# Kernel tuning notes

Measured on AMD Instinct MI355X. Metric: run time of the kernel, lower is better.

Reference implementation:

```python
import jax, jax.numpy as jnp
import numpy as np

DIM = 512
HEADS = 8
DIM_HEAD = 64
LANDMARKS = 256
PINV_ITERS = 6
RES_K = 33


def layernorm(x, g, b, eps=1e-5):
    mu = jnp.mean(x, -1, keepdims=True)
    var = jnp.mean((x - mu) ** 2, -1, keepdims=True)
    return (x - mu) / jnp.sqrt(var + eps) * g + b


def moore_penrose_pinv(x, iters=PINV_ITERS):
    abs_x = jnp.abs(x)
    col = abs_x.sum(-1)
    row = abs_x.sum(-2)
    z = jnp.swapaxes(x, -1, -2) / (jnp.max(col) * jnp.max(row))
    I = jnp.eye(x.shape[-1], dtype=x.dtype)
    for _ in range(iters):
        xz = x @ z
        z = 0.25 * z @ (13.0 * I - xz @ (15.0 * I - xz @ (7.0 * I - xz)))
    return z


def nystrom_attention(x, Wqkv, Wout, bout, res_w):
    b, n, _ = x.shape
    m = LANDMARKS
    pad = (m - n % m) % m
    if pad:
        x = jnp.pad(x, ((0, 0), (pad, 0), (0, 0)))  # front pad, as in lucidrains impl
    qkv = x @ Wqkv  # (b, np, 3*inner)
    q, k, v = jnp.split(qkv, 3, axis=-1)
    to_heads = lambda t: t.reshape(b, -1, HEADS, DIM_HEAD).transpose(0, 2, 1, 3)
    q, k, v = to_heads(q), to_heads(k), to_heads(v)  # (b,h,np,d)
    q = q * (DIM_HEAD ** -0.5)
    l = -(-n // m)  # ceil(n/m), tokens per landmark
    ql = q.reshape(b, HEADS, m, l, DIM_HEAD).sum(3) / l  # (b,h,m,d)
    kl = k.reshape(b, HEADS, m, l, DIM_HEAD).sum(3) / l
    sim1 = jnp.einsum('bhid,bhjd->bhij', q, kl)   # (b,h,np,m)
    sim2 = jnp.einsum('bhid,bhjd->bhij', ql, kl)  # (b,h,m,m)
    sim3 = jnp.einsum('bhid,bhjd->bhij', ql, k)   # (b,h,m,np)
    a1 = jax.nn.softmax(sim1, -1)
    a2 = jax.nn.softmax(sim2, -1)
    a3 = jax.nn.softmax(sim3, -1)
    a2_inv = moore_penrose_pinv(a2)
    out = (a1 @ a2_inv) @ (a3 @ v)  # (b,h,np,d)
    # depthwise residual conv along sequence (kernel 33x1, groups=heads, no bias)
    res = jax.lax.conv_general_dilated(
        v, res_w, (1, 1), [(RES_K // 2, RES_K // 2), (0, 0)],
        dimension_numbers=('NCHW', 'OIHW', 'NCHW'), feature_group_count=HEADS)
    out = out + res
    out = out.transpose(0, 2, 1, 3).reshape(b, -1, HEADS * DIM_HEAD)
    out = out @ Wout + bout
    return out[:, -n:]


def depthwise2d(x, w, b, pad):
    y = jax.lax.conv_general_dilated(
        x, w, (1, 1), [(pad, pad), (pad, pad)],
        dimension_numbers=('NCHW', 'OIHW', 'NCHW'), feature_group_count=DIM)
    return y + b[None, :, None, None]


def ppeg(x, H, W, w7, b7, w5, b5, w3, b3):
    B, _, C = x.shape
    cls_tok, feat = x[:, :1], x[:, 1:]
    cnn = feat.transpose(0, 2, 1).reshape(B, C, H, W)
    y = depthwise2d(cnn, w7, b7, 3) + cnn + depthwise2d(cnn, w5, b5, 2) + depthwise2d(cnn, w3, b3, 1)
    y = y.reshape(B, C, H * W).transpose(0, 2, 1)
    return jnp.concatenate([cls_tok, y], axis=1)


def setup_inputs() -> dict:
    key = jax.random.key(0)
    ks = jax.random.split(key, 20)
    s = 0.02
    n_classes = 5
    inp = {
        'data': jax.random.normal(ks[0], (1, 15000, 1024), jnp.float32),
        'W_fc1': jax.random.normal(ks[1], (1024, DIM), jnp.float32) * s,
        'b_fc1': jnp.zeros((DIM,), jnp.float32),
        'cls_token': jax.random.normal(ks[2], (1, 1, DIM), jnp.float32),
        'ln1_g': jnp.ones((DIM,), jnp.float32), 'ln1_b': jnp.zeros((DIM,), jnp.float32),
        'qkv1': jax.random.normal(ks[3], (DIM, 3 * HEADS * DIM_HEAD), jnp.float32) * s,
        'out1_w': jax.random.normal(ks[4], (HEADS * DIM_HEAD, DIM), jnp.float32) * s,
        'out1_b': jnp.zeros((DIM,), jnp.float32),
        'res1': jax.random.normal(ks[5], (HEADS, 1, RES_K, 1), jnp.float32) * s,
        'w7': jax.random.normal(ks[6], (DIM, 1, 7, 7), jnp.float32) * s,
        'b7': jnp.zeros((DIM,), jnp.float32),
        'w5': jax.random.normal(ks[7], (DIM, 1, 5, 5), jnp.float32) * s,
        'b5': jnp.zeros((DIM,), jnp.float32),
        'w3': jax.random.normal(ks[8], (DIM, 1, 3, 3), jnp.float32) * s,
        'b3': jnp.zeros((DIM,), jnp.float32),
        'ln2_g': jnp.ones((DIM,), jnp.float32), 'ln2_b': jnp.zeros((DIM,), jnp.float32),
        'qkv2': jax.random.normal(ks[9], (DIM, 3 * HEADS * DIM_HEAD), jnp.float32) * s,
        'out2_w': jax.random.normal(ks[10], (HEADS * DIM_HEAD, DIM), jnp.float32) * s,
        'out2_b': jnp.zeros((DIM,), jnp.float32),
        'res2': jax.random.normal(ks[11], (HEADS, 1, RES_K, 1), jnp.float32) * s,
        'norm_g': jnp.ones((DIM,), jnp.float32), 'norm_b': jnp.zeros((DIM,), jnp.float32),
        'W_fc2': jax.random.normal(ks[12], (DIM, n_classes), jnp.float32) * s,
        'b_fc2': jnp.zeros((n_classes,), jnp.float32),
    }
    return inp


def reference(data, W_fc1, b_fc1, cls_token, ln1_g, ln1_b, qkv1, out1_w, out1_b, res1,
              w7, b7, w5, b5, w3, b3, ln2_g, ln2_b, qkv2, out2_w, out2_b, res2,
              norm_g, norm_b, W_fc2, b_fc2):
    h = jax.nn.relu(data @ W_fc1 + b_fc1)  # (B, N, 512)
    N = h.shape[1]
    _H = int(np.ceil(np.sqrt(N)))
    _W = _H
    add = _H * _W - N
    h = jnp.concatenate([h, h[:, :add]], axis=1)  # pad to square grid
    B = h.shape[0]
    h = jnp.concatenate([jnp.broadcast_to(cls_token, (B, 1, DIM)), h], axis=1)
    h = h + nystrom_attention(layernorm(h, ln1_g, ln1_b), qkv1, out1_w, out1_b, res1)
    h = ppeg(h, _H, _W, w7, b7, w5, b5, w3, b3)
    h = h + nystrom_attention(layernorm(h, ln2_g, ln2_b), qkv2, out2_w, out2_b, res2)
    h = layernorm(h, norm_g, norm_b)[:, 0]
    logits = h @ W_fc2 + b_fc2
    Y_prob = jax.nn.softmax(logits, -1)
    Y_hat = jnp.argmax(logits, -1)
    return logits, Y_prob, Y_hat
```

## Files before the change

### kernel.cpp

```cpp
#include <hip/hip_runtime.h>
#include <math.h>

#define NP 15360
#define NPQ 15488
#define NTOK 15130
#define HG 123

typedef __attribute__((ext_vector_type(8))) short s8b;
typedef __attribute__((ext_vector_type(4))) float f4;

__device__ inline float bf2f(ushort u) { return __uint_as_float(((unsigned)u) << 16); }
__device__ inline ushort f2bf(float f) {
    unsigned u = __float_as_uint(f);
    unsigned r = (u + 0x7fffu + ((u >> 16) & 1u)) >> 16;
    return (ushort)r;
}

__global__ __launch_bounds__(256)
void gemm_f32(const float* __restrict__ A, int lda, long sA,
              const float* __restrict__ B, int ldb, long sB,
              float* __restrict__ C, int ldc, long sC,
              int M, int N, int K,
              const float* __restrict__ bias,
              const float* __restrict__ E, int ldE, long sE, float eS,
              float cS, int relu, int accum)
{
    A += (long)blockIdx.z * sA;
    B += (long)blockIdx.z * sB;
    C += (long)blockIdx.z * sC;
    if (E) E += (long)blockIdx.z * sE;
    const int m0 = blockIdx.y * 64, n0 = blockIdx.x * 64;
    const int t = threadIdx.x;
    const int tx = t & 15, ty = t >> 4;
    __shared__ float As[16][64];
    __shared__ float Bs[16][64];
    float acc[4][4] = {};
    const int arow = t >> 2, akc = (t & 3) * 4;
    const int brow = t >> 4, bnc = (t & 15) * 4;
    for (int k0 = 0; k0 < K; k0 += 16) {
        float4 av = make_float4(0.f, 0.f, 0.f, 0.f);
        if (m0 + arow < M) av = *(const float4*)(A + (long)(m0 + arow) * lda + k0 + akc);
        As[akc + 0][arow] = av.x; As[akc + 1][arow] = av.y;
        As[akc + 2][arow] = av.z; As[akc + 3][arow] = av.w;
        float4 bv = *(const float4*)(B + (long)(k0 + brow) * ldb + n0 + bnc);
        *(float4*)&Bs[brow][bnc] = bv;
        __syncthreads();
#pragma unroll
        for (int kk = 0; kk < 16; ++kk) {
            float4 a4 = *(const float4*)&As[kk][ty * 4];
            float4 b4 = *(const float4*)&Bs[kk][tx * 4];
            float a[4] = {a4.x, a4.y, a4.z, a4.w};
            float b[4] = {b4.x, b4.y, b4.z, b4.w};
#pragma unroll
            for (int i = 0; i < 4; i++)
#pragma unroll
                for (int j = 0; j < 4; j++) acc[i][j] = fmaf(a[i], b[j], acc[i][j]);
        }
        __syncthreads();
    }
#pragma unroll
    for (int i = 0; i < 4; i++) {
        int m = m0 + ty * 4 + i;
        if (m < M) {
#pragma unroll
            for (int j = 0; j < 4; j++) {
                int n = n0 + tx * 4 + j;
                float v = cS * acc[i][j];
                if (E) v = fmaf(eS, E[(long)m * ldE + n], v);
                if (bias) v += bias[n];
                if (relu) v = fmaxf(v, 0.f);
                if (accum) C[(long)m * ldc + n] += v;
                else C[(long)m * ldc + n] = v;
            }
        }
    }
}

template<int MT, int NT, int WROWS, int WCOLS>
__global__ __launch_bounds__(256)
void gemm_mfma(const ushort* __restrict__ A, int lda, long sA,
               const ushort* __restrict__ Bt, int ldb, long sB,
               float* __restrict__ C, int ldc, long sC,
               int M, int K,
               const float* __restrict__ bias, int relu, int accum)
{
    constexpr int TM = MT * 16 * WROWS;
    constexpr int TN = NT * 16 * WCOLS;
    constexpr int BKP = 40;
    constexpr int AIT = TM / 64;
    constexpr int BIT = TN / 64;
    __shared__ ushort As[TM * BKP];
    __shared__ ushort Bs[TN * BKP];
    A  += (long)blockIdx.z * sA;
    Bt += (long)blockIdx.z * sB;
    C  += (long)blockIdx.z * sC;
    const int t = threadIdx.x;
    const int nwg = gridDim.x * gridDim.y;
    const int flat = blockIdx.y * gridDim.x + blockIdx.x;
    const int q8 = nwg >> 3, r8 = nwg & 7;
    const int xcd = flat & 7, idx = flat >> 3;
    const int swz = (xcd < r8) ? (xcd * (q8 + 1) + idx)
                               : (r8 * (q8 + 1) + (xcd - r8) * q8 + idx);
    const int m0 = (swz / gridDim.x) * TM;
    const int n0 = (swz % gridDim.x) * TN;
    const int w = t >> 6, l = t & 63;
    const int wm = (w / WCOLS) * (MT * 16), wn = (w % WCOLS) * (NT * 16);
    const int lr = l & 15;
    const int lk = (l >> 4) * 8;
    const int srow = t >> 2, skc = (t & 3) * 8;
    f4 acc[MT][NT] = {};
    s8b pa[AIT], pb[BIT];
#pragma unroll
    for (int i = 0; i < AIT; i++)
        pa[i] = *(const s8b*)(A + (long)(m0 + srow + i * 64) * lda + skc);
#pragma unroll
    for (int i = 0; i < BIT; i++)
        pb[i] = *(const s8b*)(Bt + (long)(n0 + srow + i * 64) * ldb + skc);
    for (int k0 = 0; k0 < K; k0 += 32) {
        __syncthreads();
#pragma unroll
        for (int i = 0; i < AIT; i++)
            *(s8b*)(&As[(srow + i * 64) * BKP + skc]) = pa[i];
#pragma unroll
        for (int i = 0; i < BIT; i++)
            *(s8b*)(&Bs[(srow + i * 64) * BKP + skc]) = pb[i];
        if (k0 + 32 < K) {
#pragma unroll
            for (int i = 0; i < AIT; i++)
                pa[i] = *(const s8b*)(A + (long)(m0 + srow + i * 64) * lda + k0 + 32 + skc);
#pragma unroll
            for (int i = 0; i < BIT; i++)
                pb[i] = *(const s8b*)(Bt + (long)(n0 + srow + i * 64) * ldb + k0 + 32 + skc);
        }
        __syncthreads();
        s8b af[MT], bf[NT];
#pragma unroll
        for (int i = 0; i < MT; i++) af[i] = *(const s8b*)(&As[(wm + i * 16 + lr) * BKP + lk]);
#pragma unroll
        for (int j = 0; j < NT; j++) bf[j] = *(const s8b*)(&Bs[(wn + j * 16 + lr) * BKP + lk]);
#pragma unroll
        for (int i = 0; i < MT; i++)
#pragma unroll
            for (int j = 0; j < NT; j++)
                acc[i][j] = __builtin_amdgcn_mfma_f32_16x16x32_bf16(af[i], bf[j], acc[i][j], 0, 0, 0);
    }
    const int orow = (l >> 4) * 4;
#pragma unroll
    for (int i = 0; i < MT; i++) {
#pragma unroll
        for (int r = 0; r < 4; r++) {
            int m = m0 + wm + i * 16 + orow + r;
            if (m < M) {
#pragma unroll
                for (int j = 0; j < NT; j++) {
                    int n = n0 + wn + j * 16 + lr;
                    float vv = acc[i][j][r];
                    if (bias) vv += bias[n];
                    if (relu) vv = fmaxf(vv, 0.f);
                    if (accum) C[(long)m * ldc + n] += vv;
                    else C[(long)m * ldc + n] = vv;
                }
            }
        }
    }
}

__global__ __launch_bounds__(256)
void gemm_nn16(const ushort* __restrict__ A, const ushort* __restrict__ B,
               const ushort* __restrict__ E, ushort* __restrict__ C,
               int N, int K, float cS, float eS, long sAB)
{
    __shared__ ushort As[64 * 40];
    __shared__ ushort Bs[64 * 40];
    A += (long)blockIdx.z * sAB;
    B += (long)blockIdx.z * sAB;
    if (E) E += (long)blockIdx.z * sAB;
    C += (long)blockIdx.z * sAB;
    const int t = threadIdx.x;
    const int m0 = blockIdx.y * 64, n0 = blockIdx.x * 64;
    const int w = t >> 6, l = t & 63;
    const int wm = (w >> 1) * 32, wn = (w & 1) * 32;
    const int lr = l & 15, lk = (l >> 4) * 8;
    f4 acc[2][2] = {};
    for (int k0 = 0; k0 < K; k0 += 32) {
        {
            int row = t >> 2, kc = (t & 3) * 8;
            s8b v = *(const s8b*)(A + (long)(m0 + row) * K + k0 + kc);
            *(s8b*)(&As[row * 40 + kc]) = v;
            int kk = t >> 3, nc = (t & 7) * 8;
            s8b vb = *(const s8b*)(B + (long)(k0 + kk) * N + n0 + nc);
#pragma unroll
            for (int j = 0; j < 8; j++) Bs[(nc + j) * 40 + kk] = ((ushort*)&vb)[j];
        }
        __syncthreads();
        s8b af[2], bf[2];
#pragma unroll
        for (int i = 0; i < 2; i++) af[i] = *(const s8b*)(&As[(wm + i * 16 + lr) * 40 + lk]);
#pragma unroll
        for (int j = 0; j < 2; j++) bf[j] = *(const s8b*)(&Bs[(wn + j * 16 + lr) * 40 + lk]);
#pragma unroll
        for (int i = 0; i < 2; i++)
#pragma unroll
            for (int j = 0; j < 2; j++)
                acc[i][j] = __builtin_amdgcn_mfma_f32_16x16x32_bf16(af[i], bf[j], acc[i][j], 0, 0, 0);
        __syncthreads();
    }
    const int orow = (l >> 4) * 4;
#pragma unroll
    for (int i = 0; i < 2; i++)
#pragma unroll
        for (int r = 0; r < 4; r++) {
            int m = m0 + wm + i * 16 + orow + r;
#pragma unroll
            for (int j = 0; j < 2; j++) {
                int n = n0 + wn + j * 16 + lr;
                float vv = cS * acc[i][j][r];
                if (E) vv = fmaf(eS, bf2f(E[(long)m * N + n]), vv);
                C[(long)m * N + n] = f2bf(vv);
            }
        }
}

__global__ __launch_bounds__(256)
void gemm_qkv_mfma(const ushort* __restrict__ A, const ushort* __restrict__ Bt,
                   ushort* __restrict__ qo, ushort* __restrict__ ko, ushort* __restrict__ vo)
{
    constexpr int BKP = 40;
    __shared__ ushort As[128 * BKP];
    __shared__ ushort Bs[128 * BKP];
    const int t = threadIdx.x;
    const int nwg = gridDim.x * gridDim.y;
    const int flat = blockIdx.y * gridDim.x + blockIdx.x;
    const int q8 = nwg >> 3, r8 = nwg & 7;
    const int xcd = flat & 7, idx = flat >> 3;
    const int swz = (xcd < r8) ? (xcd * (q8 + 1) + idx)
                               : (r8 * (q8 + 1) + (xcd - r8) * q8 + idx);
    const int m0 = (swz / gridDim.x) * 128;
    const int n0 = (swz % gridDim.x) * 128;
    const int w = t >> 6, l = t & 63;
    const int wm = (w >> 1) * 64, wn = (w & 1) * 64;
    const int lr = l & 15;
    const int lk = (l >> 4) * 8;
    const int srow = t >> 2, skc = (t & 3) * 8;
    f4 acc[4][4] = {};
    s8b pa[2], pb[2];
#pragma unroll
    for (int i = 0; i < 2; i++) {
        pa[i] = *(const s8b*)(A + (long)(m0 + srow + i * 64) * 512 + skc);
        pb[i] = *(const s8b*)(Bt + (long)(n0 + srow + i * 64) * 512 + skc);
    }
    for (int k0 = 0; k0 < 512; k0 += 32) {
        __syncthreads();
#pragma unroll
        for (int i = 0; i < 2; i++) {
            *(s8b*)(&As[(srow + i * 64) * BKP + skc]) = pa[i];
            *(s8b*)(&Bs[(srow + i * 64) * BKP + skc]) = pb[i];
        }
        if (k0 + 32 < 512) {
#pragma unroll
            for (int i = 0; i < 2; i++) {
                pa[i] = *(const s8b*)(A + (long)(m0 + srow + i * 64) * 512 + k0 + 32 + skc);
                pb[i] = *(const s8b*)(Bt + (long)(n0 + srow + i * 64) * 512 + k0 + 32 + skc);
            }
        }
        __syncthreads();
        s8b af[4], bf[4];
#pragma unroll
        for (int i = 0; i < 4; i++) af[i] = *(const s8b*)(&As[(wm + i * 16 + lr) * BKP + lk]);
#pragma unroll
        for (int j = 0; j < 4; j++) bf[j] = *(const s8b*)(&Bs[(wn + j * 16 + lr) * BKP + lk]);
#pragma unroll
        for (int i = 0; i < 4; i++)
#pragma unroll
            for (int j = 0; j < 4; j++)
                acc[i][j] = __builtin_amdgcn_mfma_f32_16x16x32_bf16(af[i], bf[j], acc[i][j], 0, 0, 0);
    }
    const int orow = (l >> 4) * 4;
#pragma unroll
    for (int i = 0; i < 4; i++) {
#pragma unroll
        for (int r = 0; r < 4; r++) {
            int m = m0 + wm + i * 16 + orow + r;
#pragma unroll
            for (int j = 0; j < 4; j++) {
                int col = n0 + wn + j * 16 + lr;
                int which = col >> 9, h = (col >> 6) & 7, d = col & 63;
                float vv = acc[i][j][r];
                if (which == 0) vv *= 0.125f;
                ushort* dst = which == 0 ? qo : (which == 1 ? ko : vo);
                dst[((long)h * NPQ + m) * 64 + d] = f2bf(vv);
            }
        }
    }
}

__global__ __launch_bounds__(256, 3)
void k_flash_a3v(const ushort* __restrict__ qlb, const ushort* __restrict__ kg,
                 const ushort* __restrict__ vg,
                 float* __restrict__ pacc, float* __restrict__ pml)
{
    const int c = blockIdx.x;
    const int qt = blockIdx.y;
    const int h = blockIdx.z;
    const int t = threadIdx.x;
    const int w = t >> 6, lane = t & 63;
    const int quad = lane >> 4, l16 = lane & 15;
    const s8b vones = {0x3F80, 0x3F80, 0x3F80, 0x3F80, 0x3F80, 0x3F80, 0x3F80, 0x3F80};

    __shared__ union {
        struct { ushort Vt[64][40]; ushort Ps[128][40]; } s;
        float Os[128][68];
    } L;

    s8b aq[2][2];
    const ushort* qbase = qlb + ((long)h * 256 + qt * 128 + w * 32) * 64;
#pragma unroll
    for (int mi = 0; mi < 2; mi++)
#pragma unroll
        for (int kf = 0; kf < 2; kf++)
            aq[mi][kf] = *(const s8b*)(qbase + (mi * 16 + l16) * 64 + kf * 32 + quad * 8);

    f4 oacc[2][4] = {};
    f4 lacc[2] = {};

    const ushort* kh = kg + (long)h * NPQ * 64;
    const ushort* vh = vg + (long)h * NPQ * 64;
    const int key0c = c * 256;

    const int vkk = (t >> 3) & 31;
    const int vdc = (t & 7) * 8;
    const int vcolp = (vkk + ((vdc >> 3) & 3) * 8) & 31;

    s8b vvN = *(const s8b*)(vh + (long)(key0c + vkk) * 64 + vdc);
    s8b bqN[2][2];
#pragma unroll
    for (int nj = 0; nj < 2; nj++)
#pragma unroll
        for (int kf = 0; kf < 2; kf++)
            bqN[nj][kf] = *(const s8b*)(kh + (long)(key0c + nj * 16 + l16) * 64 + kf * 32 + quad * 8);

#pragma unroll
    for (int sub = 0; sub < 8; sub++) {
        int key0 = key0c + sub * 32;
        s8b vvC = vvN;
        s8b bq[2][2];
#pragma unroll
        for (int nj = 0; nj < 2; nj++)
#pragma unroll
            for (int kf = 0; kf < 2; kf++) bq[nj][kf] = bqN[nj][kf];
        if (sub < 7) {
            vvN = *(const s8b*)(vh + (long)(key0 + 32 + vkk) * 64 + vdc);
#pragma unroll
            for (int nj = 0; nj < 2; nj++)
#pragma unroll
                for (int kf = 0; kf < 2; kf++)
                    bqN[nj][kf] = *(const s8b*)(kh + (long)(key0 + 32 + nj * 16 + l16) * 64 + kf * 32 + quad * 8);
        }
        __syncthreads();
        {
#pragma unroll
            for (int j = 0; j < 8; j++) L.s.Vt[vdc + j][vcolp] = ((ushort*)&vvC)[j];
        }
        f4 sacc[2][2] = {};
#pragma unroll
        for (int mi = 0; mi < 2; mi++)
#pragma unroll
            for (int nj = 0; nj < 2; nj++) {
                sacc[mi][nj] = __builtin_amdgcn_mfma_f32_16x16x32_bf16(aq[mi][0], bq[nj][0], sacc[mi][nj], 0, 0, 0);
                sacc[mi][nj] = __builtin_amdgcn_mfma_f32_16x16x32_bf16(aq[mi][1], bq[nj][1], sacc[mi][nj], 0, 0, 0);
            }
#pragma unroll
        for (int mi = 0; mi < 2; mi++)
#pragma unroll
            for (int r = 0; r < 4; r++) {
                int row = w * 32 + mi * 16 + quad * 4 + r;
                L.s.Ps[row][l16]      = f2bf(__expf(sacc[mi][0][r]));
                L.s.Ps[row][16 + l16] = f2bf(__expf(sacc[mi][1][r]));
            }
        __syncthreads();
        s8b ap[2], bv[4];
#pragma unroll
        for (int mi = 0; mi < 2; mi++)
            ap[mi] = *(const s8b*)(&L.s.Ps[w * 32 + mi * 16 + l16][quad * 8]);
#pragma unroll
        for (int dj = 0; dj < 4; dj++) {
            int d = dj * 16 + l16;
            int rot = (d >> 3) & 3;
            int cb = ((quad + rot) & 3) * 8;
            bv[dj] = *(const s8b*)(&L.s.Vt[d][cb]);
        }
#pragma unroll
        for (int mi = 0; mi < 2; mi++) {
#pragma unroll
            for (int dj = 0; dj < 4; dj++)
                oacc[mi][dj] = __builtin_amdgcn_mfma_f32_16x16x32_bf16(ap[mi], bv[dj], oacc[mi][dj], 0, 0, 0);
            lacc[mi] = __builtin_amdgcn_mfma_f32_16x16x32_bf16(ap[mi], vones, lacc[mi], 0, 0, 0);
        }
    }
    __syncthreads();
#pragma unroll
    for (int mi = 0; mi < 2; mi++)
#pragma unroll
        for (int dj = 0; dj < 4; dj++)
#pragma unroll
            for (int r = 0; r < 4; r++)
                L.Os[w * 32 + mi * 16 + quad * 4 + r][dj * 16 + l16] = oacc[mi][dj][r];
    long pbase = (long)(h * 60 + c);
    if (l16 == 0) {
#pragma unroll
        for (int mi = 0; mi < 2; mi++)
#pragma unroll
            for (int r = 0; r < 4; r++) {
                int i = qt * 128 + w * 32 + mi * 16 + quad * 4 + r;
                pml[pbase * 512 + i] = 0.f;
                pml[pbase * 512 + 256 + i] = lacc[mi][r];
            }
    }
    __syncthreads();
    float* pc = pacc + pbase * 16384 + qt * 128;
    int d = t >> 2, ig = t & 3;
#pragma unroll
    for (int u = 0; u < 8; u++) {
        int i0 = ig * 32 + u * 4;
        float4 v4 = make_float4(L.Os[i0][d], L.Os[i0 + 1][d], L.Os[i0 + 2][d], L.Os[i0 + 3][d]);
        *(float4*)(pc + (long)d * 256 + i0) = v4;
    }
}

__global__ __launch_bounds__(256, 3)
void k_attn1(const ushort* __restrict__ qg, const ushort* __restrict__ klb,
             const ushort* __restrict__ BmT, const ushort* __restrict__ vg,
             const float* __restrict__ rw, ushort* __restrict__ ohb)
{
    const int m0 = blockIdx.x * 128;
    const int h = blockIdx.y;
    const int t = threadIdx.x;
    const int w = t >> 6, lane = t & 63;
    const int quad = lane >> 4, l16 = lane & 15;
    const s8b vones = {0x3F80, 0x3F80, 0x3F80, 0x3F80, 0x3F80, 0x3F80, 0x3F80, 0x3F80};

    __shared__ union {
        ushort Ps[2][128][40];
        ushort Os[128][68];
    } L;
    __shared__ __attribute__((aligned(16))) ushort Vs[160][64];

    const ushort* vh = vg + (long)h * NPQ * 64;
    {
        const ushort* srcw = vh + (long)(214 + m0 + w * 40) * 64 + lane * 8;
        ushort* dstw = &Vs[w * 40][0];
#pragma unroll
        for (int it = 0; it < 5; it++)
            __builtin_amdgcn_global_load_lds(
                (const __attribute__((address_space(1))) void*)(srcw + it * 512),
                (__attribute__((address_space(3))) void*)(dstw + it * 512),
                16, 0, 0);
    }

    s8b aq[2][2];
    const ushort* qbase = qg + ((long)h * NPQ + 230 + m0 + w * 32) * 64;
#pragma unroll
    for (int mi = 0; mi < 2; mi++)
#pragma unroll
        for (int kf = 0; kf < 2; kf++)
            aq[mi][kf] = *(const s8b*)(qbase + (mi * 16 + l16) * 64 + kf * 32 + quad * 8);

    const ushort* kh = klb + (long)h * 16384;
    const ushort* bmt = BmT + (long)h * 16384;

    s8b bqN[2][2];
#pragma unroll
    for (int nj = 0; nj < 2; nj++)
#pragma unroll
        for (int kf = 0; kf < 2; kf++)
            bqN[nj][kf] = *(const s8b*)(kh + (long)(nj * 16 + l16) * 64 + kf * 32 + quad * 8);

    f4 oacc[2][4] = {};
    f4 lacc[2] = {};
#pragma unroll
    for (int sub = 0; sub < 8; sub++) {
        int key0 = sub * 32;
        s8b bq[2][2];
#pragma unroll
        for (int nj = 0; nj < 2; nj++)
#pragma unroll
            for (int kf = 0; kf < 2; kf++) bq[nj][kf] = bqN[nj][kf];
        if (sub < 7) {
#pragma unroll
            for (int nj = 0; nj < 2; nj++)
#pragma unroll
                for (int kf = 0; kf < 2; kf++)
                    bqN[nj][kf] = *(const s8b*)(kh + (long)(key0 + 32 + nj * 16 + l16) * 64 + kf * 32 + quad * 8);
        }
        s8b bv[4];
#pragma unroll
        for (int dj = 0; dj < 4; dj++)
            bv[dj] = *(const s8b*)(bmt + (long)(dj * 16 + l16) * 256 + key0 + quad * 8);
        f4 sacc[2][2] = {};
#pragma unroll
        for (int mi = 0; mi < 2; mi++)
#pragma unroll
            for (int nj = 0; nj < 2; nj++) {
                sacc[mi][nj] = __builtin_amdgcn_mfma_f32_16x16x32_bf16(aq[mi][0], bq[nj][0], sacc[mi][nj], 0, 0, 0);
                sacc[mi][nj] = __builtin_amdgcn_mfma_f32_16x16x32_bf16(aq[mi][1], bq[nj][1], sacc[mi][nj], 0, 0, 0);
            }
        int par = sub & 1;
#pragma unroll
        for (int mi = 0; mi < 2; mi++)
#pragma unroll
            for (int r = 0; r < 4; r++) {
                int row = w * 32 + mi * 16 + quad * 4 + r;
                L.Ps[par][row][l16]      = f2bf(__expf(sacc[mi][0][r]));
                L.Ps[par][row][16 + l16] = f2bf(__expf(sacc[mi][1][r]));
            }
        s8b ap[2];
#pragma unroll
        for (int mi = 0; mi < 2; mi++)
            ap[mi] = *(const s8b*)(&L.Ps[par][w * 32 + mi * 16 + l16][quad * 8]);
#pragma unroll
        for (int mi = 0; mi < 2; mi++) {
#pragma unroll
            for (int dj = 0; dj < 4; dj++)
                oacc[mi][dj] = __builtin_amdgcn_mfma_f32_16x16x32_bf16(ap[mi], bv[dj], oacc[mi][dj], 0, 0, 0);
            lacc[mi] = __builtin_amdgcn_mfma_f32_16x16x32_bf16(ap[mi], vones, lacc[mi], 0, 0, 0);
        }
    }
    __syncthreads();

    if (214 + m0 + 160 > NP) {
        for (int r = w * 32; r < w * 32 + 64 && r < 160; ++r)
            if (214 + m0 + r >= NP) Vs[r][lane] = 0;
    }

#pragma unroll
    for (int mi = 0; mi < 2; mi++)
#pragma unroll
        for (int r = 0; r < 4; r++) {
            float inv = 1.f / lacc[mi][r];
            int row = w * 32 + mi * 16 + quad * 4 + r;
#pragma unroll
            for (int dj = 0; dj < 4; dj++)
                L.Os[row][dj * 16 + l16] = f2bf(oacc[mi][dj][r] * inv);
        }
    float rwf[33];
#pragma unroll
    for (int kk = 0; kk < 33; kk++) rwf[kk] = rw[h * 33 + kk];
#pragma unroll
    for (int half = 0; half < 2; half++) {
        const int rbase = w * 32 + half * 16;
        float vr[48];
#pragma unroll
        for (int s = 0; s < 48; s++) vr[s] = bf2f(Vs[rbase + s][lane]);
        float conv[16];
#pragma unroll
        for (int i = 0; i < 16; i++) conv[i] = 0.f;
#pragma unroll
        for (int kk = 0; kk < 33; kk++) {
            float wk = rwf[kk];
#pragma unroll
            for (int i = 0; i < 16; i++) conv[i] = fmaf(wk, vr[i + kk], conv[i]);
        }
        int t0 = m0 + rbase;
#pragma unroll
        for (int i = 0; i < 16; i++) {
            int tk = t0 + i;
            if (tk < NTOK) {
                float val = bf2f(L.Os[rbase + i][lane]) + conv[i];
                ohb[(long)tk * 512 + h * 64 + lane] = f2bf(val);
            }
        }
    }
}

__global__ __launch_bounds__(256)
void k_layernorm(const float* __restrict__ h, ushort* __restrict__ xln,
                 const float* __restrict__ g, const float* __restrict__ b, int pad)
{
    int row = blockIdx.x, t = threadIdx.x;
    if (row < pad) {
        xln[(long)row * 512 + t] = 0;
        xln[(long)row * 512 + t + 256] = 0;
        return;
    }
    const float* src = h + (long)(row - pad) * 512;
    float x1 = src[t], x2 = src[t + 256];
    float s = x1 + x2, q = x1 * x1 + x2 * x2;
    __shared__ float rs[4], rq[4], st[2];
    int wid = t >> 6, lane = t & 63;
#pragma unroll
    for (int o = 32; o > 0; o >>= 1) { s += __shfl_down(s, o); q += __shfl_down(q, o); }
    if (lane == 0) { rs[wid] = s; rq[wid] = q; }
    __syncthreads();
    if (t == 0) {
        float S = rs[0] + rs[1] + rs[2] + rs[3];
        float Q = rq[0] + rq[1] + rq[2] + rq[3];
        float mean = S / 512.f;
        float var = Q / 512.f - mean * mean;
        st[0] = mean; st[1] = rsqrtf(var + 1e-5f);
    }
    __syncthreads();
    float mean = st[0], rstd = st[1];
    xln[(long)row * 512 + t] = f2bf((x1 - mean) * rstd * g[t] + b[t]);
    xln[(long)row * 512 + t + 256] = f2bf((x2 - mean) * rstd * g[t + 256] + b[t + 256]);
}

__global__ __launch_bounds__(256)
void k_padcls(float* __restrict__ hbuf, const float* __restrict__ cls)
{
    int i = blockIdx.x, t = threadIdx.x;
    if (i == 0) { hbuf[t] = cls[t]; hbuf[t + 256] = cls[t + 256]; }
    else {
        hbuf[(long)(15000 + i) * 512 + t] = hbuf[(long)i * 512 + t];
        hbuf[(long)(15000 + i) * 512 + t + 256] = hbuf[(long)i * 512 + t + 256];
    }
}

__global__ __launch_bounds__(256)
void k_wT(const float* __restrict__ Wm, ushort* __restrict__ Wt, int K, int N, long sW, long sWt)
{
    Wm += (long)blockIdx.z * sW; Wt += (long)blockIdx.z * sWt;
    __shared__ float tile[32][33];
    int tx = threadIdx.x & 31, ty = threadIdx.x >> 5;
    int n0 = blockIdx.x * 32, k0 = blockIdx.y * 32;
#pragma unroll
    for (int u = 0; u < 4; u++) tile[ty + u * 8][tx] = Wm[(long)(k0 + ty + u * 8) * N + n0 + tx];
    __syncthreads();
#pragma unroll
    for (int u = 0; u < 4; u++) Wt[(long)(n0 + ty + u * 8) * K + k0 + tx] = f2bf(tile[tx][ty + u * 8]);
}

__global__ __launch_bounds__(256)
void k_cvt(const float4* __restrict__ src, ushort4* __restrict__ dst, long n4)
{
    long i = (long)blockIdx.x * 256 + threadIdx.x;
    if (i < n4) {
        float4 v = src[i];
        ushort4 o;
        o.x = f2bf(v.x); o.y = f2bf(v.y); o.z = f2bf(v.z); o.w = f2bf(v.w);
        dst[i] = o;
    }
}

__global__ __launch_bounds__(256)
void k_b2f(const ushort4* __restrict__ src, float4* __restrict__ dst, long n4)
{
    long i = (long)blockIdx.x * 256 + threadIdx.x;
    if (i < n4) {
        ushort4 v = src[i];
        dst[i] = make_float4(bf2f(v.x), bf2f(v.y), bf2f(v.z), bf2f(v.w));
    }
}

__global__ __launch_bounds__(64)
void k_landmarks(const ushort* __restrict__ q, const ushort* __restrict__ k,
                 float* __restrict__ ql, ushort* __restrict__ qlb,
                 float* __restrict__ klT, ushort* __restrict__ klb,
                 unsigned* __restrict__ scal)
{
    int i = blockIdx.x, h = blockIdx.y, d = threadIdx.x;
    if (i == 0 && h == 0 && d == 0) { scal[0] = 0u; scal[1] = 0u; }
    long base = ((long)h * NPQ + (long)i * 60) * 64 + d;
    float sq = 0.f, sk = 0.f;
    for (int j = 0; j < 60; j++) { sq += bf2f(q[base + j * 64]); sk += bf2f(k[base + j * 64]); }
    float qv = sq / 60.f, kv = sk / 60.f;
    ql[((long)h * 256 + i) * 64 + d] = qv;
    qlb[((long)h * 256 + i) * 64 + d] = f2bf(qv);
    klT[((long)h * 64 + d) * 256 + i] = kv;
    klb[((long)h * 256 + i) * 64 + d] = f2bf(kv);
}

__global__ __launch_bounds__(256)
void k_softmax256(float* __restrict__ X, ushort* __restrict__ X16, long headStride)
{
    float* row = X + (long)blockIdx.y * headStride + (long)blockIdx.x * 256;
    int t = threadIdx.x, wid = t >> 6, lane = t & 63;
    float x = row[t];
    __shared__ float rm[4], rsum[4], fin[2];
    float m = x;
#pragma unroll
    for (int o = 32; o > 0; o >>= 1) m = fmaxf(m, __shfl_down(m, o));
    if (lane == 0) rm[wid] = m;
    __syncthreads();
    if (t == 0) fin[0] = fmaxf(fmaxf(rm[0], rm[1]), fmaxf(rm[2], rm[3]));
    __syncthreads();
    float e = __expf(x - fin[0]);
    float s = e;
#pragma unroll
    for (int o = 32; o > 0; o >>= 1) s += __shfl_down(s, o);
    if (lane == 0) rsum[wid] = s;
    __syncthreads();
    if (t == 0) fin[1] = rsum[0] + rsum[1] + rsum[2] + rsum[3];
    __syncthreads();
    float v = e / fin[1];
    row[t] = v;
    if (X16) X16[(long)blockIdx.y * headStride + (long)blockIdx.x * 256 + t] = f2bf(v);
}

__global__ __launch_bounds__(256)
void k_colmax(const float* __restrict__ a2, unsigned* __restrict__ scal)
{
    int h = blockIdx.x, t = threadIdx.x, wid = t >> 6, lane = t & 63;
    const float* A = a2 + (long)h * 65536;
    float cs = 0.f, rs = 0.f;
    for (int i = 0; i < 256; i++) cs += A[(long)i * 256 + t];
    for (int j = 0; j < 256; j++) rs += A[(long)t * 256 + j];
    __shared__ float r1[4], r2[4];
    float m1v = cs, m2v = rs;
#pragma unroll
    for (int o = 32; o > 0; o >>= 1) {
        m1v = fmaxf(m1v, __shfl_down(m1v, o));
        m2v = fmaxf(m2v, __shfl_down(m2v, o));
    }
    if (lane == 0) { r1[wid] = m1v; r2[wid] = m2v; }
    __syncthreads();
    if (t == 0) {
        float a = fmaxf(fmaxf(r1[0], r1[1]), fmaxf(r1[2], r1[3]));
        float b = fmaxf(fmaxf(r2[0], r2[1]), fmaxf(r2[2], r2[3]));
        atomicMax(scal + 0, __float_as_uint(a));
        atomicMax(scal + 1, __float_as_uint(b));
    }
}

__global__ __launch_bounds__(256)
void k_zinit(const float* __restrict__ a2, ushort* __restrict__ zb, const unsigned* __restrict__ scal)
{
    float s = 1.f / (__uint_as_float(scal[0]) * __uint_as_float(scal[1]));
    const float* A = a2 + (long)blockIdx.z * 65536;
    ushort* Z = zb + (long)blockIdx.z * 65536;
    __shared__ float tile[32][33];
    int tx = threadIdx.x & 31, ty = threadIdx.x >> 5;
    int i0 = blockIdx.x * 32, j0 = blockIdx.y * 32;
#pragma unroll
    for (int u = 0; u < 4; u++) tile[ty + u * 8][tx] = A[(long)(j0 + ty + u * 8) * 256 + i0 + tx];
    __syncthreads();
#pragma unroll
    for (int u = 0; u < 4; u++) Z[(long)(i0 + ty + u * 8) * 256 + j0 + tx] = f2bf(tile[tx][ty + u * 8] * s);
}

__global__ __launch_bounds__(256)
void k_a3v_merge(const float* __restrict__ pacc, const float* __restrict__ pml,
                 float* __restrict__ t1)
{
    int d = blockIdx.x, h = blockIdx.y, i = threadIdx.x;
    float M = -INFINITY, L = 0.f, num = 0.f;
    for (int c = 0; c < 60; c++) {
        float mc = pml[(long)(h * 60 + c) * 2 * 256 + i];
        float lc = pml[((long)(h * 60 + c) * 2 + 1) * 256 + i];
        float ac = pacc[((long)(h * 60 + c) * 64 + d) * 256 + i];
        if (mc > M) {
            float f = __expf(M - mc);
            num = num * f + ac; L = L * f + lc; M = mc;
        } else {
            float p = __expf(mc - M);
            num = fmaf(p, ac, num); L = fmaf(p, lc, L);
        }
    }
    t1[((long)h * 256 + i) * 64 + d] = num / L;
}

__global__ __launch_bounds__(256)
void k_cls(const ushort* __restrict__ qb, const float* __restrict__ klT,
           const float* __restrict__ Bm, const ushort* __restrict__ vb,
           const float* __restrict__ rw, float* __restrict__ oh)
{
    int h = blockIdx.x, t = threadIdx.x, wid = t >> 6, lane = t & 63;
    __shared__ float qs[64], p[256], red[256];
    __shared__ float rm[4], rsum[4], fin[2];
    if (t < 64) qs[t] = bf2f(qb[((long)h * NPQ + 230) * 64 + t]);
    __syncthreads();
    float s = 0.f;
    for (int d = 0; d < 64; d++) s = fmaf(qs[d], klT[((long)h * 64 + d) * 256 + t], s);
    float m = s;
#pragma unroll
    for (int o = 32; o > 0; o >>= 1) m = fmaxf(m, __shfl_down(m, o));
    if (lane == 0) rm[wid] = m;
    __syncthreads();
    if (t == 0) fin[0] = fmaxf(fmaxf(rm[0], rm[1]), fmaxf(rm[2], rm[3]));
    __syncthreads();
    float e = __expf(s - fin[0]);
    float ss = e;
#pragma unroll
    for (int o = 32; o > 0; o >>= 1) ss += __shfl_down(ss, o);
    if (lane == 0) rsum[wid] = ss;
    __syncthreads();
    if (t == 0) fin[1] = rsum[0] + rsum[1] + rsum[2] + rsum[3];
    __syncthreads();
    p[t] = e / fin[1];
    __syncthreads();
    int d = t & 63, grp = t >> 6;
    float o = 0.f;
    for (int j = grp * 64; j < grp * 64 + 64; j++) o = fmaf(p[j], Bm[((long)h * 256 + j) * 64 + d], o);
    red[t] = o;
    __syncthreads();
    if (t < 64) {
        float val = red[t] + red[t + 64] + red[t + 128] + red[t + 192];
#pragma unroll
        for (int kk = 0; kk < 33; kk++)
            val = fmaf(rw[h * 33 + kk], bf2f(vb[((long)h * NPQ + 214 + kk) * 64 + t]), val);
        oh[h * 64 + t] = val;
    }
}

__global__ __launch_bounds__(256)
void k_copy4(const float4* __restrict__ src, float4* __restrict__ dst, long n4)
{
    long i = (long)blockIdx.x * 256 + threadIdx.x;
    if (i < n4) dst[i] = src[i];
}

__global__ __launch_bounds__(512)
void k_wcomb(const float* __restrict__ w7, const float* __restrict__ b7,
             const float* __restrict__ w5, const float* __restrict__ b5,
             const float* __restrict__ w3, const float* __restrict__ b3,
             float* __restrict__ wc, float* __restrict__ bc)
{
    int k = blockIdx.x, c = threadIdx.x;
    int kr = k / 7, kc = k % 7;
    float v = w7[c * 49 + k];
    if (kr >= 1 && kr <= 5 && kc >= 1 && kc <= 5) v += w5[c * 25 + (kr - 1) * 5 + (kc - 1)];
    if (kr >= 2 && kr <= 4 && kc >= 2 && kc <= 4) v += w3[c * 9 + (kr - 2) * 3 + (kc - 2)];
    if (k == 24) v += 1.f;
    wc[k * 512 + c] = v;
    if (k == 0) bc[c] = b7[c] + b5[c] + b3[c];
}

__global__ __launch_bounds__(256, 4)
void k_ppeg4(const float* __restrict__ cnn, float* __restrict__ hbuf,
             const float* __restrict__ wc, const float* __restrict__ bc)
{
    __shared__ __attribute__((aligned(16))) float tile[320 * 32];
    const int t = threadIdx.x;
    const int w = t >> 6, lane = t & 63;
    const int c0 = blockIdx.x * 16;
    const int r0 = blockIdx.y * 8;
    const int cb = blockIdx.z * 32;
    {
        const int pl = lane >> 3;
        const int c4 = (lane & 7) * 4;
#pragma unroll
        for (int it = 0; it < 10; ++it) {
            int chunk = w * 10 + it;
            int pos = chunk * 8 + pl;
            int pr = pos / 22, pc = pos - pr * 22;
            int gr = r0 + pr - 3, gc = c0 + pc - 3;
            int grc = min(max(gr, 0), HG - 1), gcc = min(max(gc, 0), HG - 1);
            const float* src = cnn + (long)(grc * HG + gcc) * 512 + cb + c4;
            __builtin_amdgcn_global_load_lds(
                (const __attribute__((address_space(1))) void*)src,
                (__attribute__((address_space(3))) void*)(tile + chunk * 256),
                16, 0, 0);
        }
    }
    __syncthreads();
    const bool boundary = (r0 < 3) | (r0 > HG - 11) | (c0 < 3) | (c0 > HG - 19);
    if (boundary) {
        for (int pos = t; pos < 308; pos += 256) {
            int pr = pos / 22, pc = pos - pr * 22;
            int gr = r0 + pr - 3, gc = c0 + pc - 3;
            if (gr < 0 || gr >= HG || gc < 0 || gc >= HG) {
                float4 z = make_float4(0.f, 0.f, 0.f, 0.f);
#pragma unroll
                for (int c4 = 0; c4 < 32; c4 += 4) *(float4*)&tile[pos * 32 + c4] = z;
            }
        }
        __syncthreads();
    }
    const int cp = t & 15;
    const int slot = t >> 4;
    const int orow = slot >> 1;
    const int ohalf = (slot & 1) * 8;
    float a0[8], a1[8];
#pragma unroll
    for (int i = 0; i < 8; i++) { a0[i] = 0.f; a1[i] = 0.f; }
    for (int kr = 0; kr < 7; kr++) {
        float w0[14], w1[14];
        const float* trow = tile + ((orow + kr) * 22 + ohalf) * 32 + cp * 2;
#pragma unroll
        for (int j = 0; j < 14; j++) {
            float2 v = *(const float2*)(trow + j * 32);
            w0[j] = v.x; w1[j] = v.y;
        }
#pragma unroll
        for (int kc = 0; kc < 7; kc++) {
            float2 wv = *(const float2*)(wc + (long)(kr * 7 + kc) * 512 + cb + cp * 2);
#pragma unroll
            for (int i = 0; i < 8; i++) {
                a0[i] = fmaf(wv.x, w0[i + kc], a0[i]);
                a1[i] = fmaf(wv.y, w1[i + kc], a1[i]);
            }
        }
    }
    const float2 bv = *(const float2*)(bc + cb + cp * 2);
    const int gr = r0 + orow;
    if (gr < HG) {
#pragma unroll
        for (int i = 0; i < 8; i++) {
            int gc = c0 + ohalf + i;
            if (gc < HG) {
                float* dst = hbuf + (long)(1 + gr * HG + gc) * 512 + cb + cp * 2;
                dst[0] = a0[i] + bv.x;
                dst[1] = a1[i] + bv.y;
            }
        }
    }
}

__global__ __launch_bounds__(256)
void k_final(const float* __restrict__ hbuf, const float* __restrict__ g,
             const float* __restrict__ b, const float* __restrict__ W2,
             const float* __restrict__ b2, float* __restrict__ out)
{
    __shared__ float y[512];
    __shared__ float rs[4], rq[4], st[2], lg[8];
    int t = threadIdx.x, wid = t >> 6, lane = t & 63;
    float x1 = hbuf[t], x2 = hbuf[t + 256];
    float s = x1 + x2, q = x1 * x1 + x2 * x2;
#pragma unroll
    for (int o = 32; o > 0; o >>= 1) { s += __shfl_down(s, o); q += __shfl_down(q, o); }
    if (lane == 0) { rs[wid] = s; rq[wid] = q; }
    __syncthreads();
    if (t == 0) {
        float S = rs[0] + rs[1] + rs[2] + rs[3];
        float Q = rq[0] + rq[1] + rq[2] + rq[3];
        float mean = S / 512.f;
        float var = Q / 512.f - mean * mean;
        st[0] = mean; st[1] = rsqrtf(var + 1e-5f);
    }
    __syncthreads();
    float mean = st[0], rstd = st[1];
    y[t] = (x1 - mean) * rstd * g[t] + b[t];
    y[t + 256] = (x2 - mean) * rstd * g[t + 256] + b[t + 256];
    __syncthreads();
    if (t < 5) {
        float acc = b2[t];
        for (int kx = 0; kx < 512; kx++) acc = fmaf(y[kx], W2[kx * 5 + t], acc);
        lg[t] = acc;
    }
    __syncthreads();
    if (t == 0) {
        float mx = lg[0]; int am = 0;
        for (int j = 1; j < 5; j++) if (lg[j] > mx) { mx = lg[j]; am = j; }
        float e[5], se = 0.f;
        for (int j = 0; j < 5; j++) { e[j] = __expf(lg[j] - mx); se += e[j]; }
        for (int j = 0; j < 5; j++) { out[j] = lg[j]; out[5 + j] = e[j] / se; }
        out[10] = (float)am;
    }
}

extern "C" void kernel_launch(void* const* d_in, const int* in_sizes, int n_in,
                              void* d_out, int out_size, void* d_ws, size_t ws_size,
                              hipStream_t stream)
{
    const float* data  = (const float*)d_in[0];
    const float* Wfc1  = (const float*)d_in[1];
    const float* bfc1  = (const float*)d_in[2];
    const float* cls   = (const float*)d_in[3];
    const float* ln1g  = (const float*)d_in[4];
    const float* ln1b  = (const float*)d_in[5];
    const float* qkv1  = (const float*)d_in[6];
    const float* out1w = (const float*)d_in[7];
    const float* out1b = (const float*)d_in[8];
    const float* res1  = (const float*)d_in[9];
    const float* w7    = (const float*)d_in[10];
    const float* b7    = (const float*)d_in[11];
    const float* w5    = (const float*)d_in[12];
    const float* b5    = (const float*)d_in[13];
    const float* w3    = (const float*)d_in[14];
    const float* b3    = (const float*)d_in[15];
    const float* ln2g  = (const float*)d_in[16];
    const float* ln2b  = (const float*)d_in[17];
    const float* qkv2  = (const float*)d_in[18];
    const float* out2w = (const float*)d_in[19];
    const float* out2b = (const float*)d_in[20];
    const float* res2  = (const float*)d_in[21];
    const float* normg = (const float*)d_in[22];
    const float* normb = (const float*)d_in[23];
    const float* Wfc2  = (const float*)d_in[24];
    const float* bfc2  = (const float*)d_in[25];
    float* out = (float*)d_out;

    float* W = (float*)d_ws;
    size_t off = 0;
    auto alloc = [&](size_t n) { size_t o = off; off += (n + 255) & ~(size_t)255; return o; };
    float*  hbuf   = W + alloc((size_t)NTOK * 512);
    float*  ohreg  = W + alloc((size_t)15232 * 512);
    float*  oh     = ohreg;
    ushort* xln    = (ushort*)ohreg;
    ushort* qb16   = (ushort*)(W + alloc((size_t)8 * NPQ * 32));
    ushort* kb16   = (ushort*)(W + alloc((size_t)8 * NPQ * 32));
    ushort* vb16   = (ushort*)(W + alloc((size_t)8 * NPQ * 32));
    float*  ql     = W + alloc(8 * 256 * 64);
    ushort* qlb    = (ushort*)(W + alloc(8 * 256 * 32));
    float*  klT    = W + alloc(8 * 64 * 256);
    ushort* klb    = (ushort*)(W + alloc(8 * 256 * 32));
    float*  a2     = W + alloc(8 * 65536);
    ushort* a2b    = (ushort*)(W + alloc(8 * 32768));
    ushort* zb0    = (ushort*)(W + alloc(8 * 32768));
    ushort* zb1    = (ushort*)(W + alloc(8 * 32768));
    ushort* m1b    = (ushort*)(W + alloc(8 * 32768));
    ushort* mab    = (ushort*)(W + alloc(8 * 32768));
    ushort* mbb    = (ushort*)(W + alloc(8 * 32768));
    float*  z0     = W + alloc(8 * 65536);
    float*  t1     = W + alloc(8 * 256 * 64);
    float*  Bm     = W + alloc(8 * 256 * 64);
    ushort* BmbT   = (ushort*)(W + alloc(8 * 256 * 32));
    float*  scal   = W + alloc(64);
    ushort* ohb16  = (ushort*)(W + alloc((size_t)15232 * 256));
    ushort* WfcT   = (ushort*)(W + alloc(1024 * 256));
    ushort* qkv1T  = (ushort*)(W + alloc(1536 * 256));
    ushort* qkv2T  = (ushort*)(W + alloc(1536 * 256));
    ushort* out1T  = (ushort*)(W + alloc(512 * 256));
    ushort* out2T  = (ushort*)(W + alloc(512 * 256));
    float*  wc     = W + alloc(49 * 512);
    float*  bc     = W + alloc(512);
    float*  big    = W + alloc(8110080);
    ushort* datab  = (ushort*)big;
    float*  pacc   = big;
    float*  pml    = big + 7864320;
    float*  cnn    = big;
    if (ws_size < off * sizeof(float)) return;

    k_wT<<<dim3(16, 32, 1), 256, 0, stream>>>(Wfc1, WfcT, 1024, 512, 0, 0);
    k_wT<<<dim3(48, 16, 1), 256, 0, stream>>>(qkv1, qkv1T, 512, 1536, 0, 0);
    k_wT<<<dim3(48, 16, 1), 256, 0, stream>>>(qkv2, qkv2T, 512, 1536, 0, 0);
    k_wT<<<dim3(16, 16, 1), 256, 0, stream>>>(out1w, out1T, 512, 512, 0, 0);
    k_wT<<<dim3(16, 16, 1), 256, 0, stream>>>(out2w, out2T, 512, 512, 0, 0);
    k_wcomb<<<49, 512, 0, stream>>>(w7, b7, w5, b5, w3, b3, wc, bc);
    k_cvt<<<15000, 256, 0, stream>>>((const float4*)data, (ushort4*)datab, 3840000);
    gemm_mfma<2, 4, 2, 2><<<dim3(4, 235, 1), 256, 0, stream>>>(
        datab, 1024, 0, WfcT, 1024, 0, hbuf + 512, 512, 0, 15000, 1024, bfc1, 1, 0);
    k_padcls<<<130, 256, 0, stream>>>(hbuf, cls);

    auto layer = [&](const float* lng, const float* lnb, const ushort* qkvT,
                     const float* outW, const ushort* outT, const float* outB,
                     const float* resW, bool full) {
        k_layernorm<<<NP, 256, 0, stream>>>(hbuf, xln, lng, lnb, 230);
        gemm_qkv_mfma<<<dim3(12, 120, 1), 256, 0, stream>>>(xln, qkvT, qb16, kb16, vb16);
        k_landmarks<<<dim3(256, 8), 64, 0, stream>>>(qb16, kb16, ql, qlb, klT, klb, (unsigned*)scal);
        gemm_f32<<<dim3(4, 4, 8), 256, 0, stream>>>(ql, 64, 16384, klT, 256, 16384,
            a2, 256, 65536, 256, 256, 64, nullptr, nullptr, 0, 0, 0.f, 1.f, 0, 0);
        k_softmax256<<<dim3(256, 8), 256, 0, stream>>>(a2, a2b, 65536);
        k_colmax<<<8, 256, 0, stream>>>(a2, (unsigned*)scal);
        k_zinit<<<dim3(8, 8, 8), 256, 0, stream>>>(a2, zb0, (const unsigned*)scal);
        ushort* zbi = zb0; ushort* zbo = zb1;
        for (int it = 0; it < 6; ++it) {
            gemm_nn16<<<dim3(4, 4, 8), 256, 0, stream>>>(a2b, zbi, nullptr, m1b, 256, 256, 1.f, 0.f, 65536);
            gemm_nn16<<<dim3(4, 4, 8), 256, 0, stream>>>(m1b, m1b, m1b, mab, 256, 256, -1.f, 7.f, 65536);
            gemm_nn16<<<dim3(4, 4, 8), 256, 0, stream>>>(m1b, mab, m1b, mbb, 256, 256, -1.f, 15.f, 65536);
            gemm_nn16<<<dim3(4, 4, 8), 256, 0, stream>>>(zbi, mbb, zbi, zbo, 256, 256, -0.25f, 3.25f, 65536);
            ushort* tmp = zbi; zbi = zbo; zbo = tmp;
        }
        k_b2f<<<512, 256, 0, stream>>>((const ushort4*)zbi, (float4*)z0, 131072);
        k_flash_a3v<<<dim3(60, 2, 8), 256, 0, stream>>>(qlb, kb16, vb16, pacc, pml);
        k_a3v_merge<<<dim3(64, 8), 256, 0, stream>>>(pacc, pml, t1);
        gemm_f32<<<dim3(1, 4, 8), 256, 0, stream>>>(z0, 256, 65536, t1, 64, 16384,
            Bm, 64, 16384, 256, 64, 256, nullptr, nullptr, 0, 0, 0.f, 1.f, 0, 0);
        if (full) {
            k_wT<<<dim3(2, 8, 8), 256, 0, stream>>>(Bm, BmbT, 256, 64, 16384, 16384);
            k_attn1<<<dim3(119, 8), 256, 0, stream>>>(qb16, klb, BmbT, vb16, resW, ohb16);
            gemm_mfma<2, 4, 2, 2><<<dim3(4, 237, 1), 256, 0, stream>>>(
                ohb16, 512, 0, outT, 512, 0, hbuf, 512, 0, NTOK, 512, outB, 0, 1);
        } else {
            k_cls<<<8, 256, 0, stream>>>(qb16, klT, Bm, vb16, resW, oh);
            gemm_f32<<<dim3(8, 1, 1), 256, 0, stream>>>(oh, 512, 0, outW, 512, 0,
                hbuf, 512, 0, 1, 512, 512, outB, nullptr, 0, 0, 0.f, 1.f, 0, 1);
        }
    };

    layer(ln1g, ln1b, qkv1T, out1w, out1T, out1b, res1, true);
    k_copy4<<<(1936512 + 255) / 256, 256, 0, stream>>>((const float4*)(hbuf + 512), (float4*)cnn, 1936512);
    k_ppeg4<<<dim3(8, 16, 16), 256, 0, stream>>>(cnn, hbuf, wc, bc);
    layer(ln2g, ln2b, qkv2T, out2w, out2T, out2b, res2, false);
    k_final<<<1, 256, 0, stream>>>(hbuf, normg, normb, Wfc2, bfc2, out);
}
```

Baseline: 1.131 ms.

## Fuse Newton-Schulz pinv iterations into one persistent per-head kernel

Replaces 24 small batched GEMM launches per layer (6 iterations × 4 stages) with a single kernel that runs one 1024-thread workgroup per head. That workgroup computes each full 256x256 stage in turn, with block-level syncs and threadfences between stages, and prefetches the next k-slice from global memory into registers. The goal is to remove launch overhead and inter-kernel gaps. In exchange, only 8 workgroups run on a GPU with many CUs, so each stage uses far less parallelism than the old 128-block grids. After an even number of swaps the result is back in zb0, so the conversion kernel now reads zb0.

New measurement: 3.863 ms. 3.42x slower.

```diff
diff --git a/kernel.cpp b/kernel.cpp
--- a/kernel.cpp
+++ b/kernel.cpp
@@ -165,60 +165,81 @@
     }
 }
 
-__global__ __launch_bounds__(256)
-void gemm_nn16(const ushort* __restrict__ A, const ushort* __restrict__ B,
-               const ushort* __restrict__ E, ushort* __restrict__ C,
-               int N, int K, float cS, float eS, long sAB)
-{
-    __shared__ ushort As[64 * 40];
-    __shared__ ushort Bs[64 * 40];
-    A += (long)blockIdx.z * sAB;
-    B += (long)blockIdx.z * sAB;
-    if (E) E += (long)blockIdx.z * sAB;
-    C += (long)blockIdx.z * sAB;
+__device__ __forceinline__ void pinv_stage(
+    const ushort* __restrict__ A, const ushort* __restrict__ B,
+    const ushort* __restrict__ E, ushort* __restrict__ C,
+    float cS, float eS, ushort* As, ushort* Bs,
+    int t, int wm, int wn, int lr, int lk, int orow)
+{
+    const int arow = t >> 2, akc = (t & 3) * 8;
+    const int bkk = t >> 5, bnc = (t & 31) * 8;
+    f4 acc[4][4] = {};
+    s8b pa = *(const s8b*)(A + (long)arow * 256 + akc);
+    s8b pb = *(const s8b*)(B + (long)bkk * 256 + bnc);
+    for (int k0 = 0; k0 < 256; k0 += 32) {
+        __syncthreads();
+        *(s8b*)(&As[arow * 40 + akc]) = pa;
+#pragma unroll
+        for (int j = 0; j < 8; j++) Bs[(bnc + j) * 40 + bkk] = ((ushort*)&pb)[j];
+        if (k0 + 32 < 256) {
+            pa = *(const s8b*)(A + (long)arow * 256 + k0 + 32 + akc);
+            pb = *(const s8b*)(B + (long)(k0 + 32 + bkk) * 256 + bnc);
+        }
+        __syncthreads();
+        s8b af[4], bf[4];
+#pragma unroll
+        for (int i = 0; i < 4; i++) af[i] = *(const s8b*)(&As[(wm + i * 16 + lr) * 40 + lk]);
+#pragma unroll
+        for (int j = 0; j < 4; j++) bf[j] = *(const s8b*)(&Bs[(wn + j * 16 + lr) * 40 + lk]);
+#pragma unroll
+        for (int i = 0; i < 4; i++)
+#pragma unroll
+            for (int j = 0; j < 4; j++)
+                acc[i][j] = __builtin_amdgcn_mfma_f32_16x16x32_bf16(af[i], bf[j], acc[i][j], 0, 0, 0);
+    }
+#pragma unroll
+    for (int i = 0; i < 4; i++)
+#pragma unroll
+        for (int r = 0; r < 4; r++) {
+            int m = wm + i * 16 + orow + r;
+#pragma unroll
+            for (int j = 0; j < 4; j++) {
+                int n = wn + j * 16 + lr;
+                float vv = cS * acc[i][j][r];
+                if (E) vv = fmaf(eS, bf2f(E[(long)m * 256 + n]), vv);
+                C[(long)m * 256 + n] = f2bf(vv);
+            }
+        }
+    __threadfence();
+    __syncthreads();
+}
+
+__global__ __launch_bounds__(1024)
+void k_pinv(const ushort* __restrict__ a2b, ushort* __restrict__ z0,
+            ushort* __restrict__ z1, ushort* __restrict__ m1,
+            ushort* __restrict__ ma, ushort* __restrict__ mb)
+{
+    __shared__ ushort As[256 * 40];
+    __shared__ ushort Bs[256 * 40];
+    const long hs = (long)blockIdx.x * 65536;
+    const ushort* A2 = a2b + hs;
+    ushort* zin  = z0 + hs;
+    ushort* zout = z1 + hs;
+    ushort* M1 = m1 + hs;
+    ushort* MA = ma + hs;
+    ushort* MB = mb + hs;
     const int t = threadIdx.x;
-    const int m0 = blockIdx.y * 64, n0 = blockIdx.x * 64;
     const int w = t >> 6, l = t & 63;
-    const int wm = (w >> 1) * 32, wn = (w & 1) * 32;
+    const int wm = (w >> 2) * 64, wn = (w & 3) * 64;
     const int lr = l & 15, lk = (l >> 4) * 8;
-    f4 acc[2][2] = {};
-    for (int k0 = 0; k0 < K; k0 += 32) {
-        {
-            int row = t >> 2, kc = (t & 3) * 8;
-            s8b v = *(const s8b*)(A + (long)(m0 + row) * K + k0 + kc);
-            *(s8b*)(&As[row * 40 + kc]) = v;
-            int kk = t >> 3, nc = (t & 7) * 8;
-            s8b vb = *(const s8b*)(B + (long)(k0 + kk) * N + n0 + nc);
-#pragma unroll
-            for (int j = 0; j < 8; j++) Bs[(nc + j) * 40 + kk] = ((ushort*)&vb)[j];
-        }
-        __syncthreads();
-        s8b af[2], bf[2];
-#pragma unroll
-        for (int i = 0; i < 2; i++) af[i] = *(const s8b*)(&As[(wm + i * 16 + lr) * 40 + lk]);
-#pragma unroll
-        for (int j = 0; j < 2; j++) bf[j] = *(const s8b*)(&Bs[(wn + j * 16 + lr) * 40 + lk]);
-#pragma unroll
-        for (int i = 0; i < 2; i++)
-#pragma unroll
-            for (int j = 0; j < 2; j++)
-                acc[i][j] = __builtin_amdgcn_mfma_f32_16x16x32_bf16(af[i], bf[j], acc[i][j], 0, 0, 0);
-        __syncthreads();
-    }
     const int orow = (l >> 4) * 4;
-#pragma unroll
-    for (int i = 0; i < 2; i++)
-#pragma unroll
-        for (int r = 0; r < 4; r++) {
-            int m = m0 + wm + i * 16 + orow + r;
-#pragma unroll
-            for (int j = 0; j < 2; j++) {
-                int n = n0 + wn + j * 16 + lr;
-                float vv = cS * acc[i][j][r];
-                if (E) vv = fmaf(eS, bf2f(E[(long)m * N + n]), vv);
-                C[(long)m * N + n] = f2bf(vv);
-            }
-        }
+    for (int it = 0; it < 6; ++it) {
+        pinv_stage(A2,  zin, nullptr, M1,   1.f,   0.f,  As, Bs, t, wm, wn, lr, lk, orow);
+        pinv_stage(M1,  M1,  M1,     MA,   -1.f,   7.f,  As, Bs, t, wm, wn, lr, lk, orow);
+        pinv_stage(M1,  MA,  M1,     MB,   -1.f,  15.f,  As, Bs, t, wm, wn, lr, lk, orow);
+        pinv_stage(zin, MB,  zin,    zout, -0.25f, 3.25f, As, Bs, t, wm, wn, lr, lk, orow);
+        ushort* tmp = zin; zin = zout; zout = tmp;
+    }
 }
 
 __global__ __launch_bounds__(256)
@@ -1042,15 +1063,8 @@
         k_softmax256<<<dim3(256, 8), 256, 0, stream>>>(a2, a2b, 65536);
         k_colmax<<<8, 256, 0, stream>>>(a2, (unsigned*)scal);
         k_zinit<<<dim3(8, 8, 8), 256, 0, stream>>>(a2, zb0, (const unsigned*)scal);
-        ushort* zbi = zb0; ushort* zbo = zb1;
-        for (int it = 0; it < 6; ++it) {
-            gemm_nn16<<<dim3(4, 4, 8), 256, 0, stream>>>(a2b, zbi, nullptr, m1b, 256, 256, 1.f, 0.f, 65536);
-            gemm_nn16<<<dim3(4, 4, 8), 256, 0, stream>>>(m1b, m1b, m1b, mab, 256, 256, -1.f, 7.f, 65536);
-            gemm_nn16<<<dim3(4, 4, 8), 256, 0, stream>>>(m1b, mab, m1b, mbb, 256, 256, -1.f, 15.f, 65536);
-            gemm_nn16<<<dim3(4, 4, 8), 256, 0, stream>>>(zbi, mbb, zbi, zbo, 256, 256, -0.25f, 3.25f, 65536);
-            ushort* tmp = zbi; zbi = zbo; zbo = tmp;
-        }
-        k_b2f<<<512, 256, 0, stream>>>((const ushort4*)zbi, (float4*)z0, 131072);
+        k_pinv<<<8, 1024, 0, stream>>>(a2b, zb0, zb1, m1b, mab, mbb);
+        k_b2f<<<512, 256, 0, stream>>>((const ushort4*)zb0, (float4*)z0, 131072);
         k_flash_a3v<<<dim3(60, 2, 8), 256, 0, stream>>>(qlb, kb16, vb16, pacc, pml);
         k_a3v_merge<<<dim3(64, 8), 256, 0, stream>>>(pacc, pml, t1);
         gemm_f32<<<dim3(1, 4, 8), 256, 0, stream>>>(z0, 256, 65536, t1, 64, 16384,
```
